# Kernel tuning notes

Measured on AMD Instinct MI355X. Metric: run time of the kernel, lower is better.

Reference implementation:

```python
import jax, jax.numpy as jnp
import numpy as np

NE, NR = 100000, 200
STT, ABS, REL, RDIM = 512, 256, 256, 384
GAMMA = 12.0
PI = 3.141592653589793
EMB_RNG_R = float(np.sqrt(6.0 / (NR + RDIM)))
B = 8192


def setup_inputs() -> dict:
    key = jax.random.key(0)
    ks = jax.random.split(key, 16)
    cols = [
        jax.random.randint(ks[0], (B, 1), 0, NE),      # s
        jax.random.randint(ks[1], (B, 1), 0, NR),      # r
        jax.random.randint(ks[2], (B, 1), 0, NE),      # o
        jax.random.randint(ks[3], (B, 1), 0, 31),      # d
        jax.random.randint(ks[4], (B, 1), 0, 12),      # m
        jax.random.randint(ks[5], (B, 1), 0, 100),     # y
        jax.random.randint(ks[6], (B, 2 * NR), 0, 1000),  # context times
    ]
    x = jnp.concatenate(cols, axis=1).astype(jnp.int64)
    s = 0.02
    return {
        "x": x,
        "e_emb": jax.random.normal(ks[7], (NE, STT), jnp.float32) * s,
        "r_emb": jax.random.normal(ks[8], (NR, RDIM), jnp.float32) * s,
        "d_frq": jax.random.normal(ks[9], (NE, ABS), jnp.float32) * s,
        "d_phi": jax.random.normal(ks[10], (NE, ABS), jnp.float32) * s,
        "d_amp": jax.random.normal(ks[11], (NE, ABS // 2), jnp.float32) * s,
        "m_frq": jax.random.normal(ks[12], (NE, ABS), jnp.float32) * s,
        "m_phi": jax.random.normal(ks[13], (NE, ABS), jnp.float32) * s,
        "m_amp": jax.random.normal(ks[14], (NE, ABS // 2), jnp.float32) * s,
        "w_e": jax.random.normal(ks[15], (STT, REL // 2), jnp.float32) * s,
        "w_rp": jax.random.normal(jax.random.fold_in(key, 99), (NR, NR, 1), jnp.float32) * s,
    }


def _pos_emb(t):  # t: float [N] -> [N, REL]
    f = 1.0 / (10000.0 ** (jnp.arange(0, REL, 2, dtype=jnp.float32) / REL))
    rs = t[:, None] * f[None, :]
    return jnp.concatenate([jnp.cos(rs), jnp.sin(rs)], axis=1)


def reference(x, e_emb, r_emb, d_frq, d_phi, d_amp, m_frq, m_phi, m_amp, w_e, w_rp):
    f32 = jnp.float32

    def t_emb(e, d, m):  # e int [B], d,m float [B,1] -> [B, ABS]
        re_d, im_d = jnp.split(d * d_frq[e] + d_phi[e], 2, axis=1)
        ad = d_amp[e]
        demb = jnp.concatenate([ad * jnp.cos(re_d), ad * jnp.sin(im_d)], axis=1)
        re_m, im_m = jnp.split(m * m_frq[e] + m_phi[e], 2, axis=1)
        am = m_amp[e]
        memb = jnp.concatenate([am * jnp.cos(re_m), am * jnp.sin(im_m)], axis=1)
        return demb + memb

    def e_p_emb(e):  # e: [B,1,STT] -> [B,1,REL]
        re_w, im_w = jnp.split(w_e, 2, axis=0)
        re_e, im_e = jnp.split(e, 2, axis=2)
        re_p = re_e @ re_w - im_e @ im_w
        im_p = im_e @ re_w - re_e @ im_w  # note: minus, matching source
        return jnp.concatenate([re_p, im_p], axis=2)

    def e_r_emb(r_idx, e_t):  # e_t: [B,NR] float -> [B,REL,1]
        er = _pos_emb(e_t.reshape(-1)).reshape(e_t.shape[0], NR, REL)
        er = jnp.transpose(er, (0, 2, 1))  # [B,REL,NR]
        return jnp.einsum('bdn,bno->bdo', er, w_rp[r_idx])

    s_idx, r_idx, o_idx = x[:, 0], x[:, 1], x[:, 2]
    d_abs = x[:, 3:4].astype(f32)
    m_abs = x[:, 4:5].astype(f32)
    c_s = x[:, -2 * NR:-NR].astype(f32)
    c_o = x[:, -NR:].astype(f32)

    s = e_emb[s_idx][:, None, :]
    s_t = t_emb(s_idx, d_abs, m_abs)[:, None, :]
    s_p = e_p_emb(s)
    s_r = e_r_emb(r_idx, c_s)

    o = e_emb[o_idx][:, None, :]
    o_t = t_emb(o_idx, d_abs, m_abs)[:, None, :]
    o_p = e_p_emb(o)
    o_r = e_r_emb(r_idx, c_o)

    r = r_emb[r_idx][:, None, :]  # [B,1,RDIM]
    p_r = r / (EMB_RNG_R / PI)
    re_r, im_r = jnp.cos(p_r), jnp.sin(p_r)

    re_s, im_s = jnp.split(s, 2, axis=2)
    re_st, im_st = jnp.split(s_t, 2, axis=2)
    re_s = jnp.concatenate([re_s, re_st], axis=2)  # [B,1,RDIM]
    im_s = jnp.concatenate([im_s, im_st], axis=2)
    re_o, im_o = jnp.split(o, 2, axis=2)
    re_ot, im_ot = jnp.split(o_t, 2, axis=2)
    re_o = jnp.concatenate([re_o, re_ot], axis=2)
    im_o = jnp.concatenate([im_o, im_ot], axis=2)

    # RotatE complex rotation score on static+absolute part
    re_sc = re_s * re_r - im_s * im_r - re_o
    im_sc = re_s * im_r + im_s * re_r - im_o
    sc_abs = jnp.sqrt(re_sc * re_sc + im_sc * im_sc).sum(axis=2)

    # relative-time score from projected embeddings + relation-context embeddings
    s_rel = s_p + jnp.transpose(s_r, (0, 2, 1))  # [B,1,REL]
    o_rel = o_p + jnp.transpose(o_r, (0, 2, 1))
    re_sr, im_sr = jnp.split(s_rel, 2, axis=2)
    re_or, im_or = jnp.split(o_rel, 2, axis=2)
    dre, dim = re_sr - re_or, im_sr - im_or
    sc_rel = jnp.sqrt(dre * dre + dim * dim).sum(axis=2)

    return GAMMA - (sc_abs + sc_rel)  # [B,1]
```

## Files before the change

### kernel.cpp

```cpp
#include <hip/hip_runtime.h>
#include <cstdint>

#define B_ROWS 8192
#define XSTR   406
#define GAMMA_C 12.0f
#define SCALE_ANG 30.994217f

#define KH     1024
#define HPAD   1028

#define NS_BLK 4096
#define NT_BLK 128
#define NW_BLK 64
#define NPREP  (NS_BLK + NT_BLK + NW_BLK)

#define TF_BYTES    (KH*256*2)
#define WCAT_BYTES  (512*256*2)
#define SAB_BYTES   (8192*4)
#define WS_FULL     ((size_t)(TF_BYTES + WCAT_BYTES + SAB_BYTES))
#define OLDTAB_BYTES (1000*256*2)
#define WS_OLD       ((size_t)(OLDTAB_BYTES + WCAT_BYTES))

typedef __attribute__((ext_vector_type(8))) short short8v;
typedef __attribute__((ext_vector_type(4))) float float4v;

__device__ __forceinline__ float bfLo(uint32_t u) { return __uint_as_float(u << 16); }
__device__ __forceinline__ float bfHi(uint32_t u) { return __uint_as_float(u & 0xffff0000u); }
__device__ __forceinline__ float bf1(unsigned short u) { return __uint_as_float((uint32_t)u << 16); }

__device__ __forceinline__ uint32_t f2bf_u(float x) {
  uint32_t u = __float_as_uint(x);
  u += 0x7fffu + ((u >> 16) & 1u);
  return u >> 16;
}
__device__ __forceinline__ unsigned short f2bf(float x) { return (unsigned short)f2bf_u(x); }

__device__ __forceinline__ short8v cvt8(float4 a, float4 b) {
  short8v r;
  r[0] = (short)f2bf(a.x); r[1] = (short)f2bf(a.y);
  r[2] = (short)f2bf(a.z); r[3] = (short)f2bf(a.w);
  r[4] = (short)f2bf(b.x); r[5] = (short)f2bf(b.y);
  r[6] = (short)f2bf(b.z); r[7] = (short)f2bf(b.w);
  return r;
}

__global__ __launch_bounds__(256) void kge_prep3(
    const int* __restrict__ x,
    const float* __restrict__ w_e, const float* __restrict__ e_emb,
    const float* __restrict__ r_emb,
    const float* __restrict__ d_frq, const float* __restrict__ d_phi, const float* __restrict__ d_amp,
    const float* __restrict__ m_frq, const float* __restrict__ m_phi, const float* __restrict__ m_amp,
    unsigned short* __restrict__ tf, unsigned short* __restrict__ wcat,
    float* __restrict__ sabs_buf) {
  __shared__ float st2[2][2][256];
  __shared__ float redl[4];
  const int bid = blockIdx.x;
  const int tid = threadIdx.x;
  const int sub = tid >> 6, l = tid & 63;

  if (bid < NS_BLK) {
    const int rsub = tid >> 7;
    const int row = bid * 2 + rsub;
    const int j = tid & 127;
    const int* xr = x + (size_t)row * XSTR;
    const int eS = xr[0], rid = xr[1], eO = xr[2];
    const float dv = (float)xr[3], mv = (float)xr[4];
    const int j2 = 2 * j;
    #pragma unroll
    for (int ent = 0; ent < 2; ++ent) {
      const int e = ent ? eO : eS;
      float2 fd = *(const float2*)&d_frq[(size_t)e * 256 + j2];
      float2 pd = *(const float2*)&d_phi[(size_t)e * 256 + j2];
      float2 fm = *(const float2*)&m_frq[(size_t)e * 256 + j2];
      float2 pm = *(const float2*)&m_phi[(size_t)e * 256 + j2];
      const int ja = j2 & 127;
      float2 ad = *(const float2*)&d_amp[(size_t)e * 128 + ja];
      float2 am = *(const float2*)&m_amp[(size_t)e * 128 + ja];
      float a0 = fmaf(dv, fd.x, pd.x), a1 = fmaf(dv, fd.y, pd.y);
      float b0 = fmaf(mv, fm.x, pm.x), b1 = fmaf(mv, fm.y, pm.y);
      float t0, t1, u0, u1;
      if (j2 < 128) { t0 = __cosf(a0); t1 = __cosf(a1); u0 = __cosf(b0); u1 = __cosf(b1); }
      else          { t0 = __sinf(a0); t1 = __sinf(a1); u0 = __sinf(b0); u1 = __sinf(b1); }
      st2[rsub][ent][j2]     = fmaf(ad.x, t0, am.x * u0);
      st2[rsub][ent][j2 + 1] = fmaf(ad.y, t1, am.y * u1);
    }
    __syncthreads();
    const float* Es = e_emb + (size_t)eS * 512;
    const float* Eo = e_emb + (size_t)eO * 512;
    const float* Rr = r_emb + (size_t)rid * 384;
    float sabs = 0.f;
    #pragma unroll
    for (int t3 = 0; t3 < 3; ++t3) {
      const int u = t3 * 128 + j;
      float ang = Rr[u] * SCALE_ANG;
      float sr = __sinf(ang), cr = __cosf(ang);
      float res, ims, reo, imo;
      if (t3 < 2) {
        res = Es[u]; ims = Es[256 + u];
        reo = Eo[u]; imo = Eo[256 + u];
      } else {
        res = st2[rsub][0][j]; ims = st2[rsub][0][128 + j];
        reo = st2[rsub][1][j]; imo = st2[rsub][1][128 + j];
      }
      float rsc = res * cr - ims * sr - reo;
      float isc = res * sr + ims * cr - imo;
      sabs += sqrtf(rsc * rsc + isc * isc);
    }
    #pragma unroll
    for (int off = 32; off > 0; off >>= 1) sabs += __shfl_down(sabs, off);
    if (l == 0) redl[sub] = sabs;
    __syncthreads();
    if (j == 0) sabs_buf[row] = redl[2 * rsub] + redl[2 * rsub + 1];
  } else if (bid < NS_BLK + NT_BLK) {
    const int fragid = (bid - NS_BLK) * 4 + sub;
    const int kt = fragid >> 4, nt = fragid & 15;
    const int c = nt * 16 + (l & 15);
    const float f = exp2f(-(float)(c & 127) * (13.287712379549449f / 128.f));
    __align__(16) unsigned short v[8];
    #pragma unroll
    for (int jj = 0; jj < 8; ++jj) {
      int k = kt * 32 + ((l >> 4) << 3) + jj;
      float val = 0.f;
      if (k < 1000) {
        float s, cv;
        sincosf((float)k * f, &s, &cv);
        val = (c < 128) ? cv : s;
      }
      v[jj] = f2bf(val);
    }
    ((uint4*)tf)[fragid * 64 + l] = *(const uint4*)v;
  } else {
    const int fragid = (bid - NS_BLK - NT_BLK) * 4 + sub;
    const int kk = fragid >> 4, nt = fragid & 15;
    const int c = nt * 16 + (l & 15);
    __align__(16) unsigned short v[8];
    #pragma unroll
    for (int jj = 0; jj < 8; ++jj) {
      int k = kk * 32 + ((l >> 4) << 3) + jj;
      float s = (k < 256) ? 1.f : -1.f;
      float val = (c < 128) ? s * w_e[k * 128 + c]
                            : -s * w_e[(k ^ 256) * 128 + (c - 128)];
      v[jj] = f2bf(val);
    }
    ((uint4*)wcat)[fragid * 64 + l] = *(const uint4*)v;
  }
}

__global__ __launch_bounds__(256) void kge_fused5(
    const int* __restrict__ x, const float* __restrict__ e_emb,
    const float* __restrict__ w_rp,
    const unsigned short* __restrict__ wcat, const unsigned short* __restrict__ tf,
    const float* __restrict__ sabs_buf, float* __restrict__ out) {
  __shared__ __align__(16) float lds_f[16 * HPAD];
  __shared__ float prel[4][16];
  const int tid = threadIdx.x;
  const int w = tid >> 6, l = tid & 63;
  const int m0 = blockIdx.x * 16;

  #pragma unroll
  for (int i = tid; i < 16 * HPAD / 4; i += 256)
    ((float4*)lds_f)[i] = (float4){0, 0, 0, 0};
  __syncthreads();

  {
    const int hr = tid >> 4, sub16 = tid & 15;
    const int row = m0 + hr;
    const int* xr = x + (size_t)row * XSTR;
    const int rid = xr[1];
    const int* cp = xr + 6;
    const float* wp = w_rp + (size_t)rid * 200;
    float* hrow = lds_f + hr * HPAD;
    for (int n = sub16; n < 200; n += 16) {
      float wv = wp[n];
      atomicAdd(&hrow[cp[n]], wv);
      atomicAdd(&hrow[cp[200 + n]], -wv);
    }
  }

  const int rowA = m0 + (l & 15);
  const int* xrA = x + (size_t)rowA * XSTR;
  const float* Esp = e_emb + (size_t)xrA[0] * 512 + ((l >> 4) << 3);
  const float* Eop = e_emb + (size_t)xrA[2] * 512 + ((l >> 4) << 3);
  const short8v* wq = (const short8v*)wcat;
  const short8v* tq = (const short8v*)tf;

  float4v acc[16];
  #pragma unroll
  for (int i = 0; i < 16; ++i) acc[i] = (float4v){0, 0, 0, 0};

  #pragma unroll
  for (int kt = 4 * w; kt < 4 * w + 4; ++kt) {
    float4 s0 = *(const float4*)(Esp + kt * 32);
    float4 s1 = *(const float4*)(Esp + kt * 32 + 4);
    float4 o0 = *(const float4*)(Eop + kt * 32);
    float4 o1 = *(const float4*)(Eop + kt * 32 + 4);
    float4 d0 = {s0.x - o0.x, s0.y - o0.y, s0.z - o0.z, s0.w - o0.w};
    float4 d1 = {s1.x - o1.x, s1.y - o1.y, s1.z - o1.z, s1.w - o1.w};
    short8v a = cvt8(d0, d1);
    const short8v* bsrc = wq + (size_t)kt * 1024;
    #pragma unroll
    for (int nt = 0; nt < 16; ++nt)
      acc[nt] = __builtin_amdgcn_mfma_f32_16x16x32_bf16(a, bsrc[nt * 64 + l], acc[nt], 0, 0, 0);
  }
  __syncthreads();

  {
    const float* hbase = lds_f + (l & 15) * HPAD + ((l >> 4) << 3);
    #pragma unroll
    for (int g = 8 * w; g < 8 * w + 8; ++g) {
      float4 h0 = *(const float4*)(hbase + g * 32);
      float4 h1 = *(const float4*)(hbase + g * 32 + 4);
      short8v a = cvt8(h0, h1);
      const short8v* bsrc = tq + (size_t)g * 1024;
      #pragma unroll
      for (int nt = 0; nt < 16; ++nt)
        acc[nt] = __builtin_amdgcn_mfma_f32_16x16x32_bf16(a, bsrc[nt * 64 + l], acc[nt], 0, 0, 0);
    }
  }
  __syncthreads();

  float* part = lds_f;
  #pragma unroll
  for (int nt = 0; nt < 16; ++nt)
    #pragma unroll
    for (int q = 0; q < 4; ++q)
      part[((w * 16 + nt) * 256) + q * 64 + l] = acc[nt][q];
  __syncthreads();

  {
    float sq[4] = {0.f, 0.f, 0.f, 0.f};
    #pragma unroll
    for (int pp = 0; pp < 2; ++pp) {
      const int p = 2 * w + pp;
      #pragma unroll
      for (int q = 0; q < 4; ++q) {
        const int idx = q * 64 + l;
        float dre = part[(0 * 16 + p) * 256 + idx] + part[(1 * 16 + p) * 256 + idx]
                  + part[(2 * 16 + p) * 256 + idx] + part[(3 * 16 + p) * 256 + idx];
        float dim = part[(0 * 16 + p + 8) * 256 + idx] + part[(1 * 16 + p + 8) * 256 + idx]
                  + part[(2 * 16 + p + 8) * 256 + idx] + part[(3 * 16 + p + 8) * 256 + idx];
        sq[q] += sqrtf(dre * dre + dim * dim);
      }
    }
    #pragma unroll
    for (int q = 0; q < 4; ++q) {
      float s = sq[q];
      s += __shfl_xor(s, 1); s += __shfl_xor(s, 2);
      s += __shfl_xor(s, 4); s += __shfl_xor(s, 8);
      if ((l & 15) == 0) prel[w][(l >> 4) * 4 + q] = s;
    }
  }
  __syncthreads();
  if (tid < 16) {
    const int r = tid;
    float srel = prel[0][r] + prel[1][r] + prel[2][r] + prel[3][r];
    out[m0 + r] = GAMMA_C - (sabs_buf[m0 + r] + srel);
  }
}

#define NTH    512
#define RPB    8
#define ERB    (2*RPB)
#define APAD   520

__global__ void kge_table_old(unsigned short* __restrict__ tab) {
  int t = blockIdx.x;
  int j = threadIdx.x;
  double f = pow(10000.0, -(double)j / 128.0);
  double ang = (double)t * f;
  int q = j >> 1, lo = j & 1;
  tab[t * 256 + 4 * q + lo]     = f2bf((float)cos(ang));
  tab[t * 256 + 4 * q + 2 + lo] = f2bf((float)sin(ang));
}

__global__ void kge_wcat_old(const float* __restrict__ w_e, unsigned short* __restrict__ wcat) {
  int bid = blockIdx.x;
  int kk = bid >> 4, nt = bid & 15;
  int l = threadIdx.x;
  __align__(16) unsigned short v[8];
  int c = nt * 16 + (l & 15);
  #pragma unroll
  for (int j = 0; j < 8; ++j) {
    int k = kk * 32 + ((l >> 4) << 3) + j;
    float s = (k < 256) ? 1.f : -1.f;
    float val = (c < 128) ? s * w_e[k * 128 + c]
                          : -s * w_e[(k ^ 256) * 128 + (c - 128)];
    v[j] = f2bf(val);
  }
  ((uint4*)wcat)[bid * 64 + l] = *(const uint4*)v;
}

__global__ __launch_bounds__(NTH, 4) void kge_main3(
    const int* __restrict__ x,
    const float* __restrict__ e_emb, const float* __restrict__ r_emb,
    const float* __restrict__ d_frq, const float* __restrict__ d_phi, const float* __restrict__ d_amp,
    const float* __restrict__ m_frq, const float* __restrict__ m_phi, const float* __restrict__ m_amp,
    const float* __restrict__ w_rp,
    const unsigned short* __restrict__ tab, const unsigned short* __restrict__ wcat,
    float* __restrict__ out) {
  __shared__ __align__(16) unsigned short A[ERB][APAD];
  __shared__ __align__(16) unsigned short stb[ERB][256];
  __shared__ __align__(16) float p[ERB][256];
  __shared__ int meta[RPB][6];

  const int tid = threadIdx.x;
  const int base_row = blockIdx.x * RPB;
  const int w = tid >> 6, l = tid & 63;

  if (tid < RPB * 6) {
    int r = tid / 6, f = tid % 6;
    meta[r][f] = x[(size_t)(base_row + r) * XSTR + f];
  }
  __syncthreads();

  for (int i = tid; i < ERB * 128; i += NTH) {
    int er = i >> 7, k4 = i & 127;
    int e = (er & 1) ? meta[er >> 1][2] : meta[er >> 1][0];
    float4 v = ((const float4*)e_emb)[(size_t)e * 128 + k4];
    uint2 pk;
    pk.x = f2bf_u(v.x) | (f2bf_u(v.y) << 16);
    pk.y = f2bf_u(v.z) | (f2bf_u(v.w) << 16);
    *(uint2*)&A[er][k4 * 4] = pk;
  }
  for (int it = tid; it < ERB * 256; it += NTH) {
    int j = it & 255, er = it >> 8, r = er >> 1;
    int e = (er & 1) ? meta[r][2] : meta[r][0];
    float dv = (float)meta[r][3], mv = (float)meta[r][4];
    size_t b256 = (size_t)e * 256 + j, b128 = (size_t)e * 128 + (j & 127);
    float argd = fmaf(dv, d_frq[b256], d_phi[b256]);
    float argm = fmaf(mv, m_frq[b256], m_phi[b256]);
    float vd = (j < 128) ? d_amp[b128] * __cosf(argd) : d_amp[b128] * __sinf(argd);
    float vm = (j < 128) ? m_amp[b128] * __cosf(argm) : m_amp[b128] * __sinf(argm);
    stb[er][j] = f2bf(vd + vm);
  }

  float s0 = 0, s1 = 0, s2 = 0, s3 = 0, o0 = 0, o1 = 0, o2 = 0, o3 = 0;
  {
    const int wu  = __builtin_amdgcn_readfirstlane(w);
    const int rid = __builtin_amdgcn_readfirstlane(meta[wu][1]);
    const int*   cp = x + (size_t)(base_row + wu) * XSTR + 6;
    const float* wp = w_rp + (size_t)rid * 200;
    const uint2* tl = ((const uint2*)tab) + l;
    #pragma unroll 2
    for (int n = 0; n < 200; ++n) {
      float wv = wp[n];
      int cS = cp[n];
      int cO = cp[200 + n];
      uint2 qs = tl[(size_t)cS * 64];
      uint2 qo = tl[(size_t)cO * 64];
      s0 = fmaf(wv, bfLo(qs.x), s0); s1 = fmaf(wv, bfHi(qs.x), s1);
      s2 = fmaf(wv, bfLo(qs.y), s2); s3 = fmaf(wv, bfHi(qs.y), s3);
      o0 = fmaf(wv, bfLo(qo.x), o0); o1 = fmaf(wv, bfHi(qo.x), o1);
      o2 = fmaf(wv, bfLo(qo.y), o2); o3 = fmaf(wv, bfHi(qo.y), o3);
    }
  }
  __syncthreads();

  {
    float4v acc0 = {0, 0, 0, 0}, acc1 = {0, 0, 0, 0};
    const int nt0 = 2 * w, nt1 = 2 * w + 1;
    const short8v* bp = (const short8v*)wcat;
    const unsigned short* arow = &A[l & 15][(l >> 4) << 3];
    #pragma unroll 8
    for (int kk = 0; kk < 16; ++kk) {
      short8v a  = *(const short8v*)(arow + kk * 32);
      short8v b0 = bp[(kk * 16 + nt0) * 64 + l];
      short8v b1 = bp[(kk * 16 + nt1) * 64 + l];
      acc0 = __builtin_amdgcn_mfma_f32_16x16x32_bf16(a, b0, acc0, 0, 0, 0);
      acc1 = __builtin_amdgcn_mfma_f32_16x16x32_bf16(a, b1, acc1, 0, 0, 0);
    }
    int col = l & 15, rbase = (l >> 4) * 4;
    #pragma unroll
    for (int q = 0; q < 4; ++q) {
      p[rbase + q][nt0 * 16 + col] = acc0[q];
      p[rbase + q][nt1 * 16 + col] = acc1[q];
    }
  }
  __syncthreads();

  {
    int es = 2 * w, eo = 2 * w + 1;
    p[es][2 * l] += s0; p[es][2 * l + 1] += s1;
    p[es][128 + 2 * l] += s2; p[es][129 + 2 * l] += s3;
    p[eo][2 * l] += o0; p[eo][2 * l + 1] += o1;
    p[eo][128 + 2 * l] += o2; p[eo][129 + 2 * l] += o3;
  }
  __syncthreads();

  {
    int r = w;
    int rid = meta[r][1];
    float sabs = 0.f;
    #pragma unroll
    for (int u0 = 0; u0 < 384; u0 += 64) {
      int u = u0 + l;
      float ang = r_emb[(size_t)rid * 384 + u] * SCALE_ANG;
      float sr = __sinf(ang), cr = __cosf(ang);
      float res, ims, reo, imo;
      if (u < 256) {
        res = bf1(A[2 * r][u]);       ims = bf1(A[2 * r][256 + u]);
        reo = bf1(A[2 * r + 1][u]);   imo = bf1(A[2 * r + 1][256 + u]);
      } else {
        int uu = u - 256;
        res = bf1(stb[2 * r][uu]);     ims = bf1(stb[2 * r][128 + uu]);
        reo = bf1(stb[2 * r + 1][uu]); imo = bf1(stb[2 * r + 1][128 + uu]);
      }
      float rsc = res * cr - ims * sr - reo;
      float isc = res * sr + ims * cr - imo;
      sabs += sqrtf(rsc * rsc + isc * isc);
    }
    float srel = 0.f;
    #pragma unroll
    for (int u0 = 0; u0 < 128; u0 += 64) {
      int u = u0 + l;
      float dre = p[2 * r][u] - p[2 * r + 1][u];
      float dim = p[2 * r][128 + u] - p[2 * r + 1][128 + u];
      srel += sqrtf(dre * dre + dim * dim);
    }
    float tot = sabs + srel;
    #pragma unroll
    for (int off = 32; off > 0; off >>= 1) tot += __shfl_down(tot, off);
    if (l == 0) out[base_row + r] = GAMMA_C - tot;
  }
}

extern "C" void kernel_launch(void* const* d_in, const int* in_sizes, int n_in,
                              void* d_out, int out_size, void* d_ws, size_t ws_size,
                              hipStream_t stream) {
  (void)in_sizes; (void)n_in; (void)out_size;
  const int*   x     = (const int*)d_in[0];
  const float* e_emb = (const float*)d_in[1];
  const float* r_emb = (const float*)d_in[2];
  const float* d_frq = (const float*)d_in[3];
  const float* d_phi = (const float*)d_in[4];
  const float* d_amp = (const float*)d_in[5];
  const float* m_frq = (const float*)d_in[6];
  const float* m_phi = (const float*)d_in[7];
  const float* m_amp = (const float*)d_in[8];
  const float* w_e   = (const float*)d_in[9];
  const float* w_rp  = (const float*)d_in[10];
  float* out = (float*)d_out;

  if (ws_size >= WS_FULL) {
    char* base = (char*)d_ws;
    unsigned short* tf    = (unsigned short*)base;
    unsigned short* wcat  = (unsigned short*)(base + TF_BYTES);
    float*          sabsb = (float*)(base + TF_BYTES + WCAT_BYTES);
    kge_prep3<<<dim3(NPREP), dim3(256), 0, stream>>>(
        x, w_e, e_emb, r_emb, d_frq, d_phi, d_amp, m_frq, m_phi, m_amp,
        tf, wcat, sabsb);
    kge_fused5<<<dim3(B_ROWS / 16), dim3(256), 0, stream>>>(
        x, e_emb, w_rp, wcat, tf, sabsb, out);
  } else if (ws_size >= WS_OLD) {
    unsigned short* tab  = (unsigned short*)d_ws;
    unsigned short* wcat = (unsigned short*)((char*)d_ws + OLDTAB_BYTES);
    kge_table_old<<<dim3(1000), dim3(128), 0, stream>>>(tab);
    kge_wcat_old<<<dim3(256), dim3(64), 0, stream>>>(w_e, wcat);
    kge_main3<<<dim3(B_ROWS / RPB), dim3(NTH), 0, stream>>>(
        x, e_emb, r_emb, d_frq, d_phi, d_amp, m_frq, m_phi, m_amp, w_rp,
        tab, wcat, out);
  }
}
```

Measured before the change: 59.30 us.

## Run absolute and relative score blocks concurrently in one merged kernel

Restructures the launch schedule. A small prep kernel now builds only the time table and the concatenated weight matrix. A single merged kernel then runs the MFMA relative-score blocks and the per-row absolute-score blocks side by side, each adding its partial into a zero-initialised output with atomics. The aim is to overlap the gather-heavy absolute work with the tensor-core relative work and to drop the intermediate sabs buffer. In exchange it adds a memset launch, output atomics, and a larger LDS footprint for the absolute blocks, which may reduce their occupancy.

```diff
diff --git a/kernel.cpp b/kernel.cpp
--- a/kernel.cpp
+++ b/kernel.cpp
@@ -9,15 +9,15 @@
 #define KH     1024
 #define HPAD   1028
 
-#define NS_BLK 4096
 #define NT_BLK 128
 #define NW_BLK 64
-#define NPREP  (NS_BLK + NT_BLK + NW_BLK)
+#define NF_BLK 512
+#define NS_BLK 4096
+#define NMRG   (NF_BLK + NS_BLK)
 
 #define TF_BYTES    (KH*256*2)
 #define WCAT_BYTES  (512*256*2)
-#define SAB_BYTES   (8192*4)
-#define WS_FULL     ((size_t)(TF_BYTES + WCAT_BYTES + SAB_BYTES))
+#define WS_FULL     ((size_t)(TF_BYTES + WCAT_BYTES))
 #define OLDTAB_BYTES (1000*256*2)
 #define WS_OLD       ((size_t)(OLDTAB_BYTES + WCAT_BYTES))
 
@@ -44,21 +44,166 @@
   return r;
 }
 
-__global__ __launch_bounds__(256) void kge_prep3(
-    const int* __restrict__ x,
-    const float* __restrict__ w_e, const float* __restrict__ e_emb,
+__global__ __launch_bounds__(256) void kge_prep0(
+    const float* __restrict__ w_e,
+    unsigned short* __restrict__ tf, unsigned short* __restrict__ wcat) {
+  const int bid = blockIdx.x;
+  const int tid = threadIdx.x;
+  const int sub = tid >> 6, l = tid & 63;
+  if (bid < NT_BLK) {
+    const int fragid = bid * 4 + sub;
+    const int kt = fragid >> 4, nt = fragid & 15;
+    const int c = nt * 16 + (l & 15);
+    const float f = exp2f(-(float)(c & 127) * (13.287712379549449f / 128.f));
+    __align__(16) unsigned short v[8];
+    #pragma unroll
+    for (int jj = 0; jj < 8; ++jj) {
+      int k = kt * 32 + ((l >> 4) << 3) + jj;
+      float val = 0.f;
+      if (k < 1000) {
+        float s, cv;
+        sincosf((float)k * f, &s, &cv);
+        val = (c < 128) ? cv : s;
+      }
+      v[jj] = f2bf(val);
+    }
+    ((uint4*)tf)[fragid * 64 + l] = *(const uint4*)v;
+  } else {
+    const int fragid = (bid - NT_BLK) * 4 + sub;
+    const int kk = fragid >> 4, nt = fragid & 15;
+    const int c = nt * 16 + (l & 15);
+    __align__(16) unsigned short v[8];
+    #pragma unroll
+    for (int jj = 0; jj < 8; ++jj) {
+      int k = kk * 32 + ((l >> 4) << 3) + jj;
+      float s = (k < 256) ? 1.f : -1.f;
+      float val = (c < 128) ? s * w_e[k * 128 + c]
+                            : -s * w_e[(k ^ 256) * 128 + (c - 128)];
+      v[jj] = f2bf(val);
+    }
+    ((uint4*)wcat)[fragid * 64 + l] = *(const uint4*)v;
+  }
+}
+
+__global__ __launch_bounds__(256) void kge_merged(
+    const int* __restrict__ x, const float* __restrict__ e_emb,
     const float* __restrict__ r_emb,
     const float* __restrict__ d_frq, const float* __restrict__ d_phi, const float* __restrict__ d_amp,
     const float* __restrict__ m_frq, const float* __restrict__ m_phi, const float* __restrict__ m_amp,
-    unsigned short* __restrict__ tf, unsigned short* __restrict__ wcat,
-    float* __restrict__ sabs_buf) {
+    const float* __restrict__ w_rp,
+    const unsigned short* __restrict__ wcat, const unsigned short* __restrict__ tf,
+    float* __restrict__ out) {
+  __shared__ __align__(16) float lds_f[16 * HPAD];
   __shared__ float st2[2][2][256];
   __shared__ float redl[4];
-  const int bid = blockIdx.x;
+  __shared__ float prel[4][16];
   const int tid = threadIdx.x;
-  const int sub = tid >> 6, l = tid & 63;
-
-  if (bid < NS_BLK) {
+  const int w = tid >> 6, l = tid & 63;
+
+  if (blockIdx.x < NF_BLK) {
+    const int m0 = blockIdx.x * 16;
+
+    #pragma unroll
+    for (int i = tid; i < 16 * HPAD / 4; i += 256)
+      ((float4*)lds_f)[i] = (float4){0, 0, 0, 0};
+    __syncthreads();
+
+    {
+      const int hr = tid >> 4, sub16 = tid & 15;
+      const int row = m0 + hr;
+      const int* xr = x + (size_t)row * XSTR;
+      const int rid = xr[1];
+      const int* cp = xr + 6;
+      const float* wp = w_rp + (size_t)rid * 200;
+      float* hrow = lds_f + hr * HPAD;
+      for (int n = sub16; n < 200; n += 16) {
+        float wv = wp[n];
+        atomicAdd(&hrow[cp[n]], wv);
+        atomicAdd(&hrow[cp[200 + n]], -wv);
+      }
+    }
+
+    const int rowA = m0 + (l & 15);
+    const int* xrA = x + (size_t)rowA * XSTR;
+    const float* Esp = e_emb + (size_t)xrA[0] * 512 + ((l >> 4) << 3);
+    const float* Eop = e_emb + (size_t)xrA[2] * 512 + ((l >> 4) << 3);
+    const short8v* wq = (const short8v*)wcat;
+    const short8v* tq = (const short8v*)tf;
+
+    float4v acc[16];
+    #pragma unroll
+    for (int i = 0; i < 16; ++i) acc[i] = (float4v){0, 0, 0, 0};
+
+    #pragma unroll
+    for (int kt = 4 * w; kt < 4 * w + 4; ++kt) {
+      float4 s0 = *(const float4*)(Esp + kt * 32);
+      float4 s1 = *(const float4*)(Esp + kt * 32 + 4);
+      float4 o0 = *(const float4*)(Eop + kt * 32);
+      float4 o1 = *(const float4*)(Eop + kt * 32 + 4);
+      float4 d0 = {s0.x - o0.x, s0.y - o0.y, s0.z - o0.z, s0.w - o0.w};
+      float4 d1 = {s1.x - o1.x, s1.y - o1.y, s1.z - o1.z, s1.w - o1.w};
+      short8v a = cvt8(d0, d1);
+      const short8v* bsrc = wq + (size_t)kt * 1024;
+      #pragma unroll
+      for (int nt = 0; nt < 16; ++nt)
+        acc[nt] = __builtin_amdgcn_mfma_f32_16x16x32_bf16(a, bsrc[nt * 64 + l], acc[nt], 0, 0, 0);
+    }
+    __syncthreads();
+
+    {
+      const float* hbase = lds_f + (l & 15) * HPAD + ((l >> 4) << 3);
+      #pragma unroll
+      for (int g = 8 * w; g < 8 * w + 8; ++g) {
+        float4 h0 = *(const float4*)(hbase + g * 32);
+        float4 h1 = *(const float4*)(hbase + g * 32 + 4);
+        short8v a = cvt8(h0, h1);
+        const short8v* bsrc = tq + (size_t)g * 1024;
+        #pragma unroll
+        for (int nt = 0; nt < 16; ++nt)
+          acc[nt] = __builtin_amdgcn_mfma_f32_16x16x32_bf16(a, bsrc[nt * 64 + l], acc[nt], 0, 0, 0);
+      }
+    }
+    __syncthreads();
+
+    float* part = lds_f;
+    #pragma unroll
+    for (int nt = 0; nt < 16; ++nt)
+      #pragma unroll
+      for (int q = 0; q < 4; ++q)
+        part[((w * 16 + nt) * 256) + q * 64 + l] = acc[nt][q];
+    __syncthreads();
+
+    {
+      float sq[4] = {0.f, 0.f, 0.f, 0.f};
+      #pragma unroll
+      for (int pp = 0; pp < 2; ++pp) {
+        const int p = 2 * w + pp;
+        #pragma unroll
+        for (int q = 0; q < 4; ++q) {
+          const int idx = q * 64 + l;
+          float dre = part[(0 * 16 + p) * 256 + idx] + part[(1 * 16 + p) * 256 + idx]
+                    + part[(2 * 16 + p) * 256 + idx] + part[(3 * 16 + p) * 256 + idx];
+          float dim = part[(0 * 16 + p + 8) * 256 + idx] + part[(1 * 16 + p + 8) * 256 + idx]
+                    + part[(2 * 16 + p + 8) * 256 + idx] + part[(3 * 16 + p + 8) * 256 + idx];
+          sq[q] += sqrtf(dre * dre + dim * dim);
+        }
+      }
+      #pragma unroll
+      for (int q = 0; q < 4; ++q) {
+        float s = sq[q];
+        s += __shfl_xor(s, 1); s += __shfl_xor(s, 2);
+        s += __shfl_xor(s, 4); s += __shfl_xor(s, 8);
+        if ((l & 15) == 0) prel[w][(l >> 4) * 4 + q] = s;
+      }
+    }
+    __syncthreads();
+    if (tid < 16) {
+      const int r = tid;
+      float srel = prel[0][r] + prel[1][r] + prel[2][r] + prel[3][r];
+      atomicAdd(&out[m0 + r], -srel);
+    }
+  } else {
+    const int bid = blockIdx.x - NF_BLK;
     const int rsub = tid >> 7;
     const int row = bid * 2 + rsub;
     const int j = tid & 127;
@@ -108,153 +253,9 @@
     }
     #pragma unroll
     for (int off = 32; off > 0; off >>= 1) sabs += __shfl_down(sabs, off);
-    if (l == 0) redl[sub] = sabs;
-    __syncthreads();
-    if (j == 0) sabs_buf[row] = redl[2 * rsub] + redl[2 * rsub + 1];
-  } else if (bid < NS_BLK + NT_BLK) {
-    const int fragid = (bid - NS_BLK) * 4 + sub;
-    const int kt = fragid >> 4, nt = fragid & 15;
-    const int c = nt * 16 + (l & 15);
-    const float f = exp2f(-(float)(c & 127) * (13.287712379549449f / 128.f));
-    __align__(16) unsigned short v[8];
-    #pragma unroll
-    for (int jj = 0; jj < 8; ++jj) {
-      int k = kt * 32 + ((l >> 4) << 3) + jj;
-      float val = 0.f;
-      if (k < 1000) {
-        float s, cv;
-        sincosf((float)k * f, &s, &cv);
-        val = (c < 128) ? cv : s;
-      }
-      v[jj] = f2bf(val);
-    }
-    ((uint4*)tf)[fragid * 64 + l] = *(const uint4*)v;
-  } else {
-    const int fragid = (bid - NS_BLK - NT_BLK) * 4 + sub;
-    const int kk = fragid >> 4, nt = fragid & 15;
-    const int c = nt * 16 + (l & 15);
-    __align__(16) unsigned short v[8];
-    #pragma unroll
-    for (int jj = 0; jj < 8; ++jj) {
-      int k = kk * 32 + ((l >> 4) << 3) + jj;
-      float s = (k < 256) ? 1.f : -1.f;
-      float val = (c < 128) ? s * w_e[k * 128 + c]
-                            : -s * w_e[(k ^ 256) * 128 + (c - 128)];
-      v[jj] = f2bf(val);
-    }
-    ((uint4*)wcat)[fragid * 64 + l] = *(const uint4*)v;
-  }
-}
-
-__global__ __launch_bounds__(256) void kge_fused5(
-    const int* __restrict__ x, const float* __restrict__ e_emb,
-    const float* __restrict__ w_rp,
-    const unsigned short* __restrict__ wcat, const unsigned short* __restrict__ tf,
-    const float* __restrict__ sabs_buf, float* __restrict__ out) {
-  __shared__ __align__(16) float lds_f[16 * HPAD];
-  __shared__ float prel[4][16];
-  const int tid = threadIdx.x;
-  const int w = tid >> 6, l = tid & 63;
-  const int m0 = blockIdx.x * 16;
-
-  #pragma unroll
-  for (int i = tid; i < 16 * HPAD / 4; i += 256)
-    ((float4*)lds_f)[i] = (float4){0, 0, 0, 0};
-  __syncthreads();
-
-  {
-    const int hr = tid >> 4, sub16 = tid & 15;
-    const int row = m0 + hr;
-    const int* xr = x + (size_t)row * XSTR;
-    const int rid = xr[1];
-    const int* cp = xr + 6;
-    const float* wp = w_rp + (size_t)rid * 200;
-    float* hrow = lds_f + hr * HPAD;
-    for (int n = sub16; n < 200; n += 16) {
-      float wv = wp[n];
-      atomicAdd(&hrow[cp[n]], wv);
-      atomicAdd(&hrow[cp[200 + n]], -wv);
-    }
-  }
-
-  const int rowA = m0 + (l & 15);
-  const int* xrA = x + (size_t)rowA * XSTR;
-  const float* Esp = e_emb + (size_t)xrA[0] * 512 + ((l >> 4) << 3);
-  const float* Eop = e_emb + (size_t)xrA[2] * 512 + ((l >> 4) << 3);
-  const short8v* wq = (const short8v*)wcat;
-  const short8v* tq = (const short8v*)tf;
-
-  float4v acc[16];
-  #pragma unroll
-  for (int i = 0; i < 16; ++i) acc[i] = (float4v){0, 0, 0, 0};
-
-  #pragma unroll
-  for (int kt = 4 * w; kt < 4 * w + 4; ++kt) {
-    float4 s0 = *(const float4*)(Esp + kt * 32);
-    float4 s1 = *(const float4*)(Esp + kt * 32 + 4);
-    float4 o0 = *(const float4*)(Eop + kt * 32);
-    float4 o1 = *(const float4*)(Eop + kt * 32 + 4);
-    float4 d0 = {s0.x - o0.x, s0.y - o0.y, s0.z - o0.z, s0.w - o0.w};
-    float4 d1 = {s1.x - o1.x, s1.y - o1.y, s1.z - o1.z, s1.w - o1.w};
-    short8v a = cvt8(d0, d1);
-    const short8v* bsrc = wq + (size_t)kt * 1024;
-    #pragma unroll
-    for (int nt = 0; nt < 16; ++nt)
-      acc[nt] = __builtin_amdgcn_mfma_f32_16x16x32_bf16(a, bsrc[nt * 64 + l], acc[nt], 0, 0, 0);
-  }
-  __syncthreads();
-
-  {
-    const float* hbase = lds_f + (l & 15) * HPAD + ((l >> 4) << 3);
-    #pragma unroll
-    for (int g = 8 * w; g < 8 * w + 8; ++g) {
-      float4 h0 = *(const float4*)(hbase + g * 32);
-      float4 h1 = *(const float4*)(hbase + g * 32 + 4);
-      short8v a = cvt8(h0, h1);
-      const short8v* bsrc = tq + (size_t)g * 1024;
-      #pragma unroll
-      for (int nt = 0; nt < 16; ++nt)
-        acc[nt] = __builtin_amdgcn_mfma_f32_16x16x32_bf16(a, bsrc[nt * 64 + l], acc[nt], 0, 0, 0);
-    }
-  }
-  __syncthreads();
-
-  float* part = lds_f;
-  #pragma unroll
-  for (int nt = 0; nt < 16; ++nt)
-    #pragma unroll
-    for (int q = 0; q < 4; ++q)
-      part[((w * 16 + nt) * 256) + q * 64 + l] = acc[nt][q];
-  __syncthreads();
-
-  {
-    float sq[4] = {0.f, 0.f, 0.f, 0.f};
-    #pragma unroll
-    for (int pp = 0; pp < 2; ++pp) {
-      const int p = 2 * w + pp;
-      #pragma unroll
-      for (int q = 0; q < 4; ++q) {
-        const int idx = q * 64 + l;
-        float dre = part[(0 * 16 + p) * 256 + idx] + part[(1 * 16 + p) * 256 + idx]
-                  + part[(2 * 16 + p) * 256 + idx] + part[(3 * 16 + p) * 256 + idx];
-        float dim = part[(0 * 16 + p + 8) * 256 + idx] + part[(1 * 16 + p + 8) * 256 + idx]
-                  + part[(2 * 16 + p + 8) * 256 + idx] + part[(3 * 16 + p + 8) * 256 + idx];
-        sq[q] += sqrtf(dre * dre + dim * dim);
-      }
-    }
-    #pragma unroll
-    for (int q = 0; q < 4; ++q) {
-      float s = sq[q];
-      s += __shfl_xor(s, 1); s += __shfl_xor(s, 2);
-      s += __shfl_xor(s, 4); s += __shfl_xor(s, 8);
-      if ((l & 15) == 0) prel[w][(l >> 4) * 4 + q] = s;
-    }
-  }
-  __syncthreads();
-  if (tid < 16) {
-    const int r = tid;
-    float srel = prel[0][r] + prel[1][r] + prel[2][r] + prel[3][r];
-    out[m0 + r] = GAMMA_C - (sabs_buf[m0 + r] + srel);
+    if (l == 0) redl[w] = sabs;
+    __syncthreads();
+    if (j == 0) atomicAdd(&out[row], GAMMA_C - (redl[2 * rsub] + redl[2 * rsub + 1]));
   }
 }
 
@@ -443,14 +444,13 @@
 
   if (ws_size >= WS_FULL) {
     char* base = (char*)d_ws;
-    unsigned short* tf    = (unsigned short*)base;
-    unsigned short* wcat  = (unsigned short*)(base + TF_BYTES);
-    float*          sabsb = (float*)(base + TF_BYTES + WCAT_BYTES);
-    kge_prep3<<<dim3(NPREP), dim3(256), 0, stream>>>(
-        x, w_e, e_emb, r_emb, d_frq, d_phi, d_amp, m_frq, m_phi, m_amp,
-        tf, wcat, sabsb);
-    kge_fused5<<<dim3(B_ROWS / 16), dim3(256), 0, stream>>>(
-        x, e_emb, w_rp, wcat, tf, sabsb, out);
+    unsigned short* tf   = (unsigned short*)base;
+    unsigned short* wcat = (unsigned short*)(base + TF_BYTES);
+    hipMemsetAsync(out, 0, (size_t)B_ROWS * sizeof(float), stream);
+    kge_prep0<<<dim3(NT_BLK + NW_BLK), dim3(256), 0, stream>>>(w_e, tf, wcat);
+    kge_merged<<<dim3(NMRG), dim3(256), 0, stream>>>(
+        x, e_emb, r_emb, d_frq, d_phi, d_amp, m_frq, m_phi, m_amp, w_rp,
+        wcat, tf, out);
   } else if (ws_size >= WS_OLD) {
     unsigned short* tab  = (unsigned short*)d_ws;
     unsigned short* wcat = (unsigned short*)((char*)d_ws + OLDTAB_BYTES);
```

Result: slower. 70.48 us (+18.8%).
